# Optimization experiments

Hardware: AMD Instinct MI355X
Metric: run time of the kernel (lower is better)

Reference implementation:

```python
import jax, jax.numpy as jnp
import numpy as np

C = 512
HEADS = 8
HEAD_DIM = 64
OUT = 2560
NEG = -1.0e12
EPS = 1e-5


def _layernorm(x, g, b):
    mu = jnp.mean(x, axis=-1, keepdims=True)
    var = jnp.mean(jnp.square(x - mu), axis=-1, keepdims=True)
    return (x - mu) * jax.lax.rsqrt(var + EPS) * g + b


def setup_inputs() -> dict:
    key = jax.random.key(0)
    ks = jax.random.split(key, 16)
    s = 0.02
    return {
        "x": jax.random.normal(ks[0], (8, C, 32, 32), dtype=jnp.float32),
        "conv_w": jax.random.normal(ks[1], (C, C), dtype=jnp.float32) * s,
        "conv_b": jnp.zeros((C,), jnp.float32),
        "ln_g": jnp.ones((C,), jnp.float32),
        "ln_b": jnp.zeros((C,), jnp.float32),
        "qkv_w": jax.random.normal(ks[2], (3 * C, C), dtype=jnp.float32) * s,
        "qkv_b": jnp.zeros((3 * C,), jnp.float32),
        "proj_w": jax.random.normal(ks[3], (C, C), dtype=jnp.float32) * s,
        "proj_b": jnp.zeros((C,), jnp.float32),
        "w1": jax.random.normal(ks[4], (C, C), dtype=jnp.float32) * s,
        "b1": jnp.zeros((C,), jnp.float32),
        "w2": jax.random.normal(ks[5], (C, C), dtype=jnp.float32) * s,
        "b2": jnp.zeros((C,), jnp.float32),
        "fc_w": jax.random.normal(ks[6], (OUT, C), dtype=jnp.float32) * s,
        "fc_b": jnp.zeros((OUT,), jnp.float32),
    }


def reference(x, conv_w, conv_b, ln_g, ln_b, qkv_w, qkv_b, proj_w, proj_b,
              w1, b1, w2, b2, fc_w, fc_b):
    B, Cc, H, W = x.shape
    N = H * W
    mk = jax.random.split(jax.random.key(42), 3)

    # Flat1D: conv1x1 == per-pixel linear, then flatten -> [B, N, C]
    t = jnp.einsum('bchw,oc->bhwo', x, conv_w) + conv_b
    t = t.reshape(B, N, Cc)

    # LayerNorm (shared params)
    t = _layernorm(t, ln_g, ln_b)

    # Attention with random additive mask (p=0.5)
    qkv = t @ qkv_w.T + qkv_b  # [B, N, 3C]
    qkv = qkv.reshape(B, N, 3, HEADS, Cc // HEADS)
    q = jnp.transpose(qkv[:, :, 0], (0, 2, 1, 3))  # [B, H, N, D]
    k = jnp.transpose(qkv[:, :, 1], (0, 2, 1, 3))
    v = jnp.transpose(qkv[:, :, 2], (0, 2, 1, 3))
    scale = HEAD_DIM ** (-0.5)
    attn = jnp.einsum('bhnd,bhmd->bhnm', q, k) * scale
    amask = jax.random.bernoulli(mk[0], 0.5, attn.shape)
    attn = attn + amask.astype(attn.dtype) * NEG
    attn = jax.nn.softmax(attn, axis=-1)
    o = jnp.einsum('bhnm,bhmd->bhnd', attn, v)
    o = jnp.transpose(o, (0, 2, 1, 3)).reshape(B, N, Cc)
    t = o @ proj_w.T + proj_b

    # FeedForward with random additive masks
    h = jax.nn.gelu(t @ w1.T + b1, approximate=False)
    m1 = jax.random.bernoulli(mk[1], 0.3, h.shape)
    h = h + m1.astype(h.dtype) * NEG
    t = h @ w2.T + b2
    m2 = jax.random.bernoulli(mk[2], 0.1, t.shape)
    t = t + m2.astype(t.dtype) * NEG

    # LayerNorm (same params), mean over tokens, final fc
    t = _layernorm(t, ln_g, ln_b)
    t = jnp.mean(t, axis=1)  # [B, C]
    return t @ fc_w.T + fc_b
```

## Files before the change

### kernel.cpp

```cpp
#include <hip/hip_runtime.h>
#include <stdint.h>
#include <math.h>

#define NEGV -1.0e12f
#define QSCALE 0.18033688011112042f

typedef __attribute__((ext_vector_type(8))) short bf16x8;
typedef __attribute__((ext_vector_type(4))) float f32x4;
typedef __attribute__((ext_vector_type(8))) ushort u16x8;

#define ROTL1(v, r) ({ uint32_t _d;                                            \
    asm("v_alignbit_b32 %0, %1, %1, %2" : "=v"(_d) : "v"(v), "n"(32 - (r)));   \
    _d; })

#if defined(__has_builtin)
#if __has_builtin(__builtin_amdgcn_exp2f)
#define EXP2(x) __builtin_amdgcn_exp2f(x)
#endif
#endif
#ifndef EXP2
#define EXP2(x) exp2f(x)
#endif

__host__ static void tf2x32_host(uint32_t k0, uint32_t k1, uint32_t c0, uint32_t c1,
                                 uint32_t* o0, uint32_t* o1) {
    uint32_t ks2 = k0 ^ k1 ^ 0x1BD11BDAu;
    uint32_t x0 = c0 + k0, x1 = c1 + k1;
#define TF_RND(r) x0 += x1; x1 = ((x1 << (r)) | (x1 >> (32 - (r)))); x1 ^= x0;
    TF_RND(13) TF_RND(15) TF_RND(26) TF_RND(6)
    x0 += k1;  x1 += ks2 + 1u;
    TF_RND(17) TF_RND(29) TF_RND(16) TF_RND(24)
    x0 += ks2; x1 += k0 + 2u;
    TF_RND(13) TF_RND(15) TF_RND(26) TF_RND(6)
    x0 += k0;  x1 += k1 + 3u;
    TF_RND(17) TF_RND(29) TF_RND(16) TF_RND(24)
    x0 += k1;  x1 += ks2 + 4u;
    TF_RND(13) TF_RND(15) TF_RND(26) TF_RND(6)
    x0 += ks2; x1 += k0 + 5u;
#undef TF_RND
    *o0 = x0; *o1 = x1;
}

__device__ __forceinline__ uint32_t tf_bits(uint32_t k0, uint32_t k1, uint32_t j) {
    const uint32_t ks2 = k0 ^ k1 ^ 0x1BD11BDAu;
    uint32_t x0 = k0, x1 = j + k1;
#define TFR(r) x0 += x1; x1 = ROTL1(x1, r); x1 ^= x0;
    TFR(13) TFR(15) TFR(26) TFR(6)
    x0 += k1;  x1 += ks2 + 1u;
    TFR(17) TFR(29) TFR(16) TFR(24)
    x0 += ks2; x1 += k0 + 2u;
    TFR(13) TFR(15) TFR(26) TFR(6)
    x0 += k0;  x1 += k1 + 3u;
    TFR(17) TFR(29) TFR(16) TFR(24)
    x0 += k1;  x1 += ks2 + 4u;
    TFR(13) TFR(15) TFR(26) TFR(6)
#undef TFR
    return (x0 + ks2) ^ (x1 + (k0 + 5u));
}

__host__ static uint32_t maskT(float p) {
    double t = ceil((double)p * 8388608.0);
    return ((uint32_t)t) << 9;
}

__device__ __forceinline__ ushort f2bf(float x) {
    uint32_t u = __float_as_uint(x);
    u += 0x7fffu + ((u >> 16) & 1u);
    return (ushort)(u >> 16);
}
__device__ __forceinline__ float bf2f(ushort u) {
    return __uint_as_float(((uint32_t)u) << 16);
}

__global__ __launch_bounds__(256) void prep_k(const float* __restrict__ x,
                                              ushort* __restrict__ xt,
                                              const float* __restrict__ s0,
                                              const float* __restrict__ s1,
                                              const float* __restrict__ s2,
                                              const float* __restrict__ s3,
                                              const float* __restrict__ s4,
                                              ushort* __restrict__ wdst)
{
    __shared__ float tile[64][65];
    const int tid = threadIdx.x;
    if (blockIdx.x < 1024) {
        const int id = blockIdx.x;
        const int n0 = (id & 15) * 64, c0 = ((id >> 4) & 7) * 64, b = id >> 7;
        const float* src = x + ((size_t)b * 512 + c0) * 1024 + n0;
#pragma unroll
        for (int i = 0; i < 4; ++i) {
            const int r = (tid >> 4) + i * 16;
            const int col = (tid & 15) * 4;
            float4 v = *(const float4*)(src + (size_t)r * 1024 + col);
            tile[r][col + 0] = v.x; tile[r][col + 1] = v.y;
            tile[r][col + 2] = v.z; tile[r][col + 3] = v.w;
        }
        __syncthreads();
#pragma unroll
        for (int i = 0; i < 2; ++i) {
            const int nl = (tid >> 3) + i * 32;
            const int cb = (tid & 7) * 8;
            u16x8 o;
#pragma unroll
            for (int j = 0; j < 8; ++j) o[j] = f2bf(tile[cb + j][nl]);
            *(u16x8*)(xt + ((size_t)b * 1024 + n0 + nl) * 512 + c0 + cb) = o;
        }
    } else {
        const size_t i = ((size_t)(blockIdx.x - 1024) * 256 + tid) * 8;
        const float* src; size_t off;
        if (i < 262144)       { src = s0; off = 0; }
        else if (i < 1048576) { src = s1; off = 262144; }
        else if (i < 1310720) { src = s2; off = 1048576; }
        else if (i < 1572864) { src = s3; off = 1310720; }
        else                  { src = s4; off = 1572864; }
        const float* p = src + (i - off);
        float4 a = *(const float4*)p;
        float4 b = *(const float4*)(p + 4);
        u16x8 o;
        o[0] = f2bf(a.x); o[1] = f2bf(a.y); o[2] = f2bf(a.z); o[3] = f2bf(a.w);
        o[4] = f2bf(b.x); o[5] = f2bf(b.y); o[6] = f2bf(b.z); o[7] = f2bf(b.w);
        *(u16x8*)(wdst + i) = o;
    }
}

template<int EPI>
__global__ __launch_bounds__(256) void bgemm_k(
    const ushort* __restrict__ A, const ushort* __restrict__ W,
    const float* __restrict__ bias, float* __restrict__ outf,
    ushort* __restrict__ outb,
    ushort* __restrict__ qb, ushort* __restrict__ kb, ushort* __restrict__ vb,
    uint32_t mkk0, uint32_t mkk1, uint32_t T)
{
    const int tid = threadIdx.x;
    const int wave = tid >> 6, lane = tid & 63;
    const int lg = lane >> 4, lc = lane & 15;
    const int m0 = blockIdx.x * 128 + wave * 32;
    const int o0 = blockIdx.y * 64;

    f32x4 acc[2][4];
#pragma unroll
    for (int i = 0; i < 2; ++i)
#pragma unroll
        for (int j = 0; j < 4; ++j) acc[i][j] = (f32x4){0.f, 0.f, 0.f, 0.f};

    const ushort* Ab = A + (size_t)(m0 + lc) * 512 + lg * 8;
    const ushort* Wb = W + (size_t)(o0 + lc) * 512 + lg * 8;

#pragma unroll 4
    for (int k0 = 0; k0 < 512; k0 += 32) {
        bf16x8 aq[2], bw[4];
        aq[0] = *(const bf16x8*)(Ab + k0);
        aq[1] = *(const bf16x8*)(Ab + 16 * 512 + k0);
#pragma unroll
        for (int j = 0; j < 4; ++j) bw[j] = *(const bf16x8*)(Wb + (size_t)j * 16 * 512 + k0);
#pragma unroll
        for (int i = 0; i < 2; ++i)
#pragma unroll
            for (int j = 0; j < 4; ++j)
                acc[i][j] = __builtin_amdgcn_mfma_f32_16x16x32_bf16(aq[i], bw[j], acc[i][j], 0, 0, 0);
    }

    float bvv[4];
#pragma unroll
    for (int j = 0; j < 4; ++j) bvv[j] = bias[o0 + j * 16 + lc];

#pragma unroll
    for (int i = 0; i < 2; ++i) {
#pragma unroll
        for (int j = 0; j < 4; ++j) {
#pragma unroll
            for (int r = 0; r < 4; ++r) {
                const int m = m0 + i * 16 + lg * 4 + r;
                const int o = o0 + j * 16 + lc;
                float v = acc[i][j][r] + bvv[j];
                if constexpr (EPI == 4) {
                    outb[(size_t)m * 512 + o] = f2bf(v);
                } else if constexpr (EPI == 2) {
                    v = 0.5f * v * (1.0f + erff(v * 0.70710678118654752f));
                    if (tf_bits(mkk0, mkk1, (uint32_t)(m * 512 + o)) < T) v += NEGV;
                    outb[(size_t)m * 512 + o] = f2bf(v);
                } else if constexpr (EPI == 3) {
                    if (tf_bits(mkk0, mkk1, (uint32_t)(m * 512 + o)) < T) v += NEGV;
                    outf[(size_t)m * 512 + o] = v;
                } else {
                    const int s = o >> 9, hh = (o >> 6) & 7, d = o & 63;
                    const int b = m >> 10, n = m & 1023;
                    const int bh = b * 8 + hh;
                    ushort* dst = (s == 0) ? qb : (s == 1) ? kb : vb;
                    const float scl = (s == 0) ? QSCALE : 1.0f;
                    dst[((size_t)bh * 1024 + n) * 64 + d] = f2bf(v * scl);
                }
            }
        }
    }
}

__global__ __launch_bounds__(256) void vxpose_k(const ushort* __restrict__ v,
                                                ushort* __restrict__ vt)
{
    __shared__ ushort tile[64][72];
    const int tid = threadIdx.x;
    const int bh = blockIdx.y, n0 = blockIdx.x * 64;
    const int row = tid >> 2, cq = (tid & 3) * 16;
    const ushort* src = v + ((size_t)bh * 1024 + n0 + row) * 64 + cq;
    *(u16x8*)&tile[row][cq] = *(const u16x8*)src;
    *(u16x8*)&tile[row][cq + 8] = *(const u16x8*)(src + 8);
    __syncthreads();
    const int d = tid >> 2, nq = (tid & 3) * 16;
    u16x8 o0v, o1v;
#pragma unroll
    for (int i = 0; i < 8; ++i) o0v[i] = tile[nq + i][d];
#pragma unroll
    for (int i = 0; i < 8; ++i) o1v[i] = tile[nq + 8 + i][d];
    ushort* dst = vt + ((size_t)bh * 64 + d) * 1024 + n0 + nq;
    *(u16x8*)dst = o0v;
    *(u16x8*)(dst + 8) = o1v;
}

__global__ __launch_bounds__(256) void ln_k(const ushort* __restrict__ in,
                                            const float* __restrict__ g,
                                            const float* __restrict__ bb,
                                            ushort* __restrict__ outb)
{
    const int wave = threadIdx.x >> 6, lane = threadIdx.x & 63;
    const size_t tok = (size_t)blockIdx.x * 4 + wave;
    const ushort* row = in + tok * 512;
    const int c0 = lane * 8;
    u16x8 vv = *(const u16x8*)(row + c0);
    float x[8];
#pragma unroll
    for (int i = 0; i < 8; i++) x[i] = bf2f(vv[i]);
    float s = 0.f;
#pragma unroll
    for (int i = 0; i < 8; i++) s += x[i];
#pragma unroll
    for (int sh = 32; sh; sh >>= 1) s += __shfl_xor(s, sh, 64);
    const float mu = s * (1.0f / 512.0f);
    float vsum = 0.f;
#pragma unroll
    for (int i = 0; i < 8; i++) { float d = x[i] - mu; vsum += d * d; }
#pragma unroll
    for (int sh = 32; sh; sh >>= 1) vsum += __shfl_xor(vsum, sh, 64);
    const float inv = 1.0f / sqrtf(vsum * (1.0f / 512.0f) + 1e-5f);
    float4 g0 = *(const float4*)(g + c0);
    float4 g1 = *(const float4*)(g + c0 + 4);
    float4 b0 = *(const float4*)(bb + c0);
    float4 b1 = *(const float4*)(bb + c0 + 4);
    float gg[8] = {g0.x, g0.y, g0.z, g0.w, g1.x, g1.y, g1.z, g1.w};
    float bv[8] = {b0.x, b0.y, b0.z, b0.w, b1.x, b1.y, b1.z, b1.w};
    u16x8 o;
#pragma unroll
    for (int i = 0; i < 8; i++) o[i] = f2bf((x[i] - mu) * inv * gg[i] + bv[i]);
    *(u16x8*)(outb + tok * 512 + c0) = o;
}

__global__ __launch_bounds__(256) void ln2mean_k(const float* __restrict__ in,
                                                 const float* __restrict__ g,
                                                 const float* __restrict__ bb,
                                                 float* __restrict__ pblock)
{
    __shared__ float rows[4][512];
    const int wave = threadIdx.x >> 6, lane = threadIdx.x & 63;
    const int b = blockIdx.x >> 8;
    const size_t tok = (size_t)b * 1024 + (blockIdx.x & 255) * 4 + wave;
    const float* row = in + tok * 512;
    const int c0 = lane * 8;
    float4 v0 = *(const float4*)(row + c0);
    float4 v1 = *(const float4*)(row + c0 + 4);
    float x[8] = {v0.x, v0.y, v0.z, v0.w, v1.x, v1.y, v1.z, v1.w};
    float s = 0.f;
#pragma unroll
    for (int i = 0; i < 8; i++) s += x[i];
#pragma unroll
    for (int sh = 32; sh; sh >>= 1) s += __shfl_xor(s, sh, 64);
    const float mu = s * (1.0f / 512.0f);
    float vsum = 0.f;
#pragma unroll
    for (int i = 0; i < 8; i++) { float d = x[i] - mu; vsum += d * d; }
#pragma unroll
    for (int sh = 32; sh; sh >>= 1) vsum += __shfl_xor(vsum, sh, 64);
    const float inv = 1.0f / sqrtf(vsum * (1.0f / 512.0f) + 1e-5f);
    float4 g0 = *(const float4*)(g + c0);
    float4 g1 = *(const float4*)(g + c0 + 4);
    float4 b0 = *(const float4*)(bb + c0);
    float4 b1 = *(const float4*)(bb + c0 + 4);
    float gg[8] = {g0.x, g0.y, g0.z, g0.w, g1.x, g1.y, g1.z, g1.w};
    float bv[8] = {b0.x, b0.y, b0.z, b0.w, b1.x, b1.y, b1.z, b1.w};
    float o[8];
#pragma unroll
    for (int i = 0; i < 8; i++) o[i] = (x[i] - mu) * inv * gg[i] + bv[i];
    *(float4*)&rows[wave][c0]     = make_float4(o[0], o[1], o[2], o[3]);
    *(float4*)&rows[wave][c0 + 4] = make_float4(o[4], o[5], o[6], o[7]);
    __syncthreads();
    const int c = threadIdx.x;
    float p0 = rows[0][c] + rows[1][c] + rows[2][c] + rows[3][c];
    float p1 = rows[0][c + 256] + rows[1][c + 256] + rows[2][c + 256] + rows[3][c + 256];
    pblock[(size_t)blockIdx.x * 512 + c] = p0;
    pblock[(size_t)blockIdx.x * 512 + c + 256] = p1;
}

__global__ __launch_bounds__(256) void mred_k(const float* __restrict__ pblock,
                                              float* __restrict__ tm)
{
    __shared__ float red[8][33];
    const int c0 = blockIdx.x * 32, b = blockIdx.y;
    const int cl = threadIdx.x & 31, jg = threadIdx.x >> 5;
    const float* p = pblock + ((size_t)b * 256 + jg * 32) * 512 + c0 + cl;
    float s = 0.f;
#pragma unroll 8
    for (int j = 0; j < 32; ++j) s += p[(size_t)j * 512];
    red[jg][cl] = s;
    __syncthreads();
    if (jg == 0) {
        float t = 0.f;
#pragma unroll
        for (int g2 = 0; g2 < 8; ++g2) t += red[g2][cl];
        tm[b * 512 + c0 + cl] = t * (1.0f / 1024.0f);
    }
}

__global__ __launch_bounds__(256) void attn_k(
    const ushort* __restrict__ qb, const ushort* __restrict__ kb,
    const ushort* __restrict__ vtb, ushort* __restrict__ ob,
    uint32_t km0, uint32_t km1)
{
    __shared__ ushort plds[4][16][40];
    const int tid = threadIdx.x;
    const int wave = tid >> 6, lane = tid & 63;
    const int bh = blockIdx.x & 63;
    const int qt = blockIdx.x >> 6;
    const int b = bh >> 3, h = bh & 7;
    const int q0 = qt * 64 + wave * 16;
    const int lg = lane >> 4, lc = lane & 15;

    const ushort* qp = qb + (size_t)bh * 65536;

    bf16x8 aq0 = *(const bf16x8*)(qp + (size_t)(q0 + lc) * 64 + lg * 8);
    bf16x8 aq1 = *(const bf16x8*)(qp + (size_t)(q0 + lc) * 64 + 32 + lg * 8);

    f32x4 zero = {0.f, 0.f, 0.f, 0.f};
    f32x4 oacc[4] = {zero, zero, zero, zero};
    float D[4] = {0.f, 0.f, 0.f, 0.f};

    uint32_t jr[4];
#pragma unroll
    for (int r = 0; r < 4; ++r)
        jr[r] = ((uint32_t)bh * 1024u + (uint32_t)(q0 + lg * 4 + r)) * 1024u + (uint32_t)lc;

    const ushort* krow = kb + (size_t)bh * 65536 + (size_t)lc * 64 + lg * 8;
    const ushort* vrow = vtb + (size_t)bh * 65536 + (size_t)lc * 1024 + lg * 8;

    for (int ch = 0; ch < 32; ++ch) {
        bf16x8 bk00 = *(const bf16x8*)(krow);
        bf16x8 bk01 = *(const bf16x8*)(krow + 32);
        bf16x8 bk10 = *(const bf16x8*)(krow + 1024);
        bf16x8 bk11 = *(const bf16x8*)(krow + 1056);

        f32x4 s0 = __builtin_amdgcn_mfma_f32_16x16x32_bf16(aq0, bk00, zero, 0, 0, 0);
        s0 = __builtin_amdgcn_mfma_f32_16x16x32_bf16(aq1, bk01, s0, 0, 0, 0);
        f32x4 s1 = __builtin_amdgcn_mfma_f32_16x16x32_bf16(aq0, bk10, zero, 0, 0, 0);
        s1 = __builtin_amdgcn_mfma_f32_16x16x32_bf16(aq1, bk11, s1, 0, 0, 0);

#pragma unroll
        for (int r = 0; r < 4; ++r) {
            const uint32_t bits0 = tf_bits(km0, km1, jr[r]);
            const uint32_t bits1 = tf_bits(km0, km1, jr[r] + 16u);
            jr[r] += 32u;
            const float pv0 = ((int)bits0 < 0) ? EXP2(s0[r]) : 0.f;
            const float pv1 = ((int)bits1 < 0) ? EXP2(s1[r]) : 0.f;
            D[r] += pv0 + pv1;
            uint32_t pk;
            asm("v_cvt_pk_bf16_f32 %0, %1, %2" : "=v"(pk) : "v"(pv0), "v"(pv1));
            plds[wave][lg * 4 + r][lc] = (ushort)pk;
            plds[wave][lg * 4 + r][lc + 16] = (ushort)(pk >> 16);
        }

        bf16x8 pa = *(const bf16x8*)&plds[wave][lc][lg * 8];

#pragma unroll
        for (int dt = 0; dt < 4; ++dt) {
            bf16x8 bv = *(const bf16x8*)(vrow + (size_t)dt * 16384);
            oacc[dt] = __builtin_amdgcn_mfma_f32_16x16x32_bf16(pa, bv, oacc[dt], 0, 0, 0);
        }
        krow += 2048;
        vrow += 32;
    }

#pragma unroll
    for (int r = 0; r < 4; ++r) {
#pragma unroll
        for (int sh = 1; sh < 16; sh <<= 1) D[r] += __shfl_xor(D[r], sh, 64);
    }

#pragma unroll
    for (int r = 0; r < 4; ++r) {
        const int q = q0 + lg * 4 + r;
        const float inv = 1.0f / D[r];
        ushort* orow = ob + ((size_t)b * 1024 + q) * 512 + h * 64;
#pragma unroll
        for (int dt = 0; dt < 4; ++dt) orow[dt * 16 + lc] = f2bf(oacc[dt][r] * inv);
    }
}

__global__ __launch_bounds__(256) void fc_k(const float* __restrict__ tm,
                                            const float* __restrict__ w,
                                            const float* __restrict__ bias,
                                            float* __restrict__ outp)
{
    const int b = blockIdx.y;
    const int o = blockIdx.x * 256 + threadIdx.x;
    const float* tr = tm + b * 512;
    const float* wr = w + (size_t)o * 512;
    float s = 0.f;
    for (int k = 0; k < 512; k += 4) {
        float4 a = *(const float4*)(tr + k);
        float4 ww = *(const float4*)(wr + k);
        s = fmaf(a.x, ww.x, s); s = fmaf(a.y, ww.y, s);
        s = fmaf(a.z, ww.z, s); s = fmaf(a.w, ww.w, s);
    }
    outp[b * 2560 + o] = s + bias[o];
}

extern "C" void kernel_launch(void* const* d_in, const int* in_sizes, int n_in,
                              void* d_out, int out_size, void* d_ws, size_t ws_size,
                              hipStream_t stream)
{
    const float* x      = (const float*)d_in[0];
    const float* conv_w = (const float*)d_in[1];
    const float* conv_b = (const float*)d_in[2];
    const float* ln_g   = (const float*)d_in[3];
    const float* ln_b   = (const float*)d_in[4];
    const float* qkv_w  = (const float*)d_in[5];
    const float* qkv_b  = (const float*)d_in[6];
    const float* proj_w = (const float*)d_in[7];
    const float* proj_b = (const float*)d_in[8];
    const float* w1     = (const float*)d_in[9];
    const float* b1     = (const float*)d_in[10];
    const float* w2     = (const float*)d_in[11];
    const float* b2     = (const float*)d_in[12];
    const float* fc_w   = (const float*)d_in[13];
    const float* fc_b   = (const float*)d_in[14];
    float* out = (float*)d_out;

    if (ws_size < (size_t)71303168) return;

    uint32_t mk0a, mk0b, mk1a, mk1b, mk2a, mk2b;
    tf2x32_host(0u, 42u, 0u, 0u, &mk0a, &mk0b);
    tf2x32_host(0u, 42u, 0u, 1u, &mk1a, &mk1b);
    tf2x32_host(0u, 42u, 0u, 2u, &mk2a, &mk2b);
    const uint32_t T_m1 = maskT(0.3f);
    const uint32_t T_m2 = maskT(0.1f);

    char* wsb = (char*)d_ws;
    ushort* xt     = (ushort*)wsb;
    ushort* wts    = (ushort*)(wsb + 8388608);
    ushort* qbuf   = (ushort*)(wsb + 12582912);
    ushort* kbuf   = (ushort*)(wsb + 20971520);
    ushort* vbuf   = (ushort*)(wsb + 29360128);
    ushort* vtbuf  = (ushort*)(wsb + 37748736);
    ushort* convbf = (ushort*)(wsb + 46137344);
    float*  t2     = (float*)(wsb + 46137344);
    ushort* ln1bf  = (ushort*)(wsb + 62914560);
    ushort* obuf   = xt;
    ushort* projbf = ln1bf;
    ushort* hbuf   = qbuf;
    float*  pblock = (float*)(wsb + 20971520);
    float*  tm     = (float*)(wsb + 25165824);

    ushort* wconv = wts;
    ushort* wqkv  = wts + 262144;
    ushort* wproj = wts + 1048576;
    ushort* ww1   = wts + 1310720;
    ushort* ww2   = wts + 1572864;

    dim3 blk(256);
    prep_k<<<dim3(1920), blk, 0, stream>>>(x, xt, conv_w, qkv_w, proj_w, w1, w2, wts);
    bgemm_k<4><<<dim3(64, 8), blk, 0, stream>>>(xt, wconv, conv_b, nullptr, convbf,
                                                nullptr, nullptr, nullptr, 0u, 0u, 0u);
    ln_k<<<dim3(2048), blk, 0, stream>>>(convbf, ln_g, ln_b, ln1bf);
    bgemm_k<1><<<dim3(64, 24), blk, 0, stream>>>(ln1bf, wqkv, qkv_b, nullptr, nullptr,
                                                 qbuf, kbuf, vbuf, 0u, 0u, 0u);
    vxpose_k<<<dim3(16, 64), blk, 0, stream>>>(vbuf, vtbuf);
    attn_k<<<dim3(1024), blk, 0, stream>>>(qbuf, kbuf, vtbuf, obuf, mk0a, mk0b);
    bgemm_k<4><<<dim3(64, 8), blk, 0, stream>>>(obuf, wproj, proj_b, nullptr, projbf,
                                                nullptr, nullptr, nullptr, 0u, 0u, 0u);
    bgemm_k<2><<<dim3(64, 8), blk, 0, stream>>>(projbf, ww1, b1, nullptr, hbuf,
                                                nullptr, nullptr, nullptr, mk1a, mk1b, T_m1);
    bgemm_k<3><<<dim3(64, 8), blk, 0, stream>>>(hbuf, ww2, b2, t2, nullptr,
                                                nullptr, nullptr, nullptr, mk2a, mk2b, T_m2);
    ln2mean_k<<<dim3(2048), blk, 0, stream>>>(t2, ln_g, ln_b, pblock);
    mred_k<<<dim3(16, 8), blk, 0, stream>>>(pblock, tm);
    fc_k<<<dim3(10, 8), blk, 0, stream>>>(tm, fc_w, fc_b, out);
}
```

Baseline: 357.5 us.

## Fuse attention, proj, FFN, second layernorm and token-mean into one kernel

```diff
diff --git a/kernel.cpp b/kernel.cpp
--- a/kernel.cpp
+++ b/kernel.cpp
@@ -126,10 +126,9 @@
 template<int EPI>
 __global__ __launch_bounds__(256) void bgemm_k(
     const ushort* __restrict__ A, const ushort* __restrict__ W,
-    const float* __restrict__ bias, float* __restrict__ outf,
+    const float* __restrict__ bias,
     ushort* __restrict__ outb,
-    ushort* __restrict__ qb, ushort* __restrict__ kb, ushort* __restrict__ vb,
-    uint32_t mkk0, uint32_t mkk1, uint32_t T)
+    ushort* __restrict__ qb, ushort* __restrict__ kb, ushort* __restrict__ vb)
 {
     const int tid = threadIdx.x;
     const int wave = tid >> 6, lane = tid & 63;
@@ -175,13 +174,6 @@
                 float v = acc[i][j][r] + bvv[j];
                 if constexpr (EPI == 4) {
                     outb[(size_t)m * 512 + o] = f2bf(v);
-                } else if constexpr (EPI == 2) {
-                    v = 0.5f * v * (1.0f + erff(v * 0.70710678118654752f));
-                    if (tf_bits(mkk0, mkk1, (uint32_t)(m * 512 + o)) < T) v += NEGV;
-                    outb[(size_t)m * 512 + o] = f2bf(v);
-                } else if constexpr (EPI == 3) {
-                    if (tf_bits(mkk0, mkk1, (uint32_t)(m * 512 + o)) < T) v += NEGV;
-                    outf[(size_t)m * 512 + o] = v;
                 } else {
                     const int s = o >> 9, hh = (o >> 6) & 7, d = o & 63;
                     const int b = m >> 10, n = m & 1023;
@@ -254,87 +246,28 @@
     *(u16x8*)(outb + tok * 512 + c0) = o;
 }
 
-__global__ __launch_bounds__(256) void ln2mean_k(const float* __restrict__ in,
-                                                 const float* __restrict__ g,
-                                                 const float* __restrict__ bb,
-                                                 float* __restrict__ pblock)
-{
-    __shared__ float rows[4][512];
-    const int wave = threadIdx.x >> 6, lane = threadIdx.x & 63;
-    const int b = blockIdx.x >> 8;
-    const size_t tok = (size_t)b * 1024 + (blockIdx.x & 255) * 4 + wave;
-    const float* row = in + tok * 512;
-    const int c0 = lane * 8;
-    float4 v0 = *(const float4*)(row + c0);
-    float4 v1 = *(const float4*)(row + c0 + 4);
-    float x[8] = {v0.x, v0.y, v0.z, v0.w, v1.x, v1.y, v1.z, v1.w};
-    float s = 0.f;
-#pragma unroll
-    for (int i = 0; i < 8; i++) s += x[i];
-#pragma unroll
-    for (int sh = 32; sh; sh >>= 1) s += __shfl_xor(s, sh, 64);
-    const float mu = s * (1.0f / 512.0f);
-    float vsum = 0.f;
-#pragma unroll
-    for (int i = 0; i < 8; i++) { float d = x[i] - mu; vsum += d * d; }
-#pragma unroll
-    for (int sh = 32; sh; sh >>= 1) vsum += __shfl_xor(vsum, sh, 64);
-    const float inv = 1.0f / sqrtf(vsum * (1.0f / 512.0f) + 1e-5f);
-    float4 g0 = *(const float4*)(g + c0);
-    float4 g1 = *(const float4*)(g + c0 + 4);
-    float4 b0 = *(const float4*)(bb + c0);
-    float4 b1 = *(const float4*)(bb + c0 + 4);
-    float gg[8] = {g0.x, g0.y, g0.z, g0.w, g1.x, g1.y, g1.z, g1.w};
-    float bv[8] = {b0.x, b0.y, b0.z, b0.w, b1.x, b1.y, b1.z, b1.w};
-    float o[8];
-#pragma unroll
-    for (int i = 0; i < 8; i++) o[i] = (x[i] - mu) * inv * gg[i] + bv[i];
-    *(float4*)&rows[wave][c0]     = make_float4(o[0], o[1], o[2], o[3]);
-    *(float4*)&rows[wave][c0 + 4] = make_float4(o[4], o[5], o[6], o[7]);
-    __syncthreads();
-    const int c = threadIdx.x;
-    float p0 = rows[0][c] + rows[1][c] + rows[2][c] + rows[3][c];
-    float p1 = rows[0][c + 256] + rows[1][c + 256] + rows[2][c + 256] + rows[3][c + 256];
-    pblock[(size_t)blockIdx.x * 512 + c] = p0;
-    pblock[(size_t)blockIdx.x * 512 + c + 256] = p1;
-}
-
-__global__ __launch_bounds__(256) void mred_k(const float* __restrict__ pblock,
-                                              float* __restrict__ tm)
-{
-    __shared__ float red[8][33];
-    const int c0 = blockIdx.x * 32, b = blockIdx.y;
-    const int cl = threadIdx.x & 31, jg = threadIdx.x >> 5;
-    const float* p = pblock + ((size_t)b * 256 + jg * 32) * 512 + c0 + cl;
-    float s = 0.f;
-#pragma unroll 8
-    for (int j = 0; j < 32; ++j) s += p[(size_t)j * 512];
-    red[jg][cl] = s;
-    __syncthreads();
-    if (jg == 0) {
-        float t = 0.f;
-#pragma unroll
-        for (int g2 = 0; g2 < 8; ++g2) t += red[g2][cl];
-        tm[b * 512 + c0 + cl] = t * (1.0f / 1024.0f);
-    }
-}
-
-__global__ __launch_bounds__(256) void attn_k(
+__global__ __launch_bounds__(512) void mega_k(
     const ushort* __restrict__ qb, const ushort* __restrict__ kb,
-    const ushort* __restrict__ vtb, ushort* __restrict__ ob,
-    uint32_t km0, uint32_t km1)
-{
-    __shared__ ushort plds[4][16][40];
+    const ushort* __restrict__ vtb,
+    const ushort* __restrict__ wproj, const float* __restrict__ pjb,
+    const ushort* __restrict__ ww1, const float* __restrict__ b1v,
+    const ushort* __restrict__ ww2, const float* __restrict__ b2v,
+    const float* __restrict__ g, const float* __restrict__ bln,
+    float* __restrict__ pblock,
+    uint32_t km0, uint32_t km1, uint32_t k10, uint32_t k11,
+    uint32_t k20, uint32_t k21, uint32_t T1, uint32_t T2)
+{
+    __shared__ ushort bufA[16][520];
+    __shared__ ushort plds[8][16][40];
+    __shared__ float stats[16][8][2];
     const int tid = threadIdx.x;
     const int wave = tid >> 6, lane = tid & 63;
-    const int bh = blockIdx.x & 63;
-    const int qt = blockIdx.x >> 6;
-    const int b = bh >> 3, h = bh & 7;
-    const int q0 = qt * 64 + wave * 16;
     const int lg = lane >> 4, lc = lane & 15;
+    const int b = blockIdx.x & 7, tg = blockIdx.x >> 3;
+    const int bh = b * 8 + wave;
+    const int q0 = tg * 16;
 
     const ushort* qp = qb + (size_t)bh * 65536;
-
     bf16x8 aq0 = *(const bf16x8*)(qp + (size_t)(q0 + lc) * 64 + lg * 8);
     bf16x8 aq1 = *(const bf16x8*)(qp + (size_t)(q0 + lc) * 64 + 32 + lg * 8);
 
@@ -394,12 +327,166 @@
 
 #pragma unroll
     for (int r = 0; r < 4; ++r) {
-        const int q = q0 + lg * 4 + r;
+        const int row = lg * 4 + r;
         const float inv = 1.0f / D[r];
-        ushort* orow = ob + ((size_t)b * 1024 + q) * 512 + h * 64;
-#pragma unroll
-        for (int dt = 0; dt < 4; ++dt) orow[dt * 16 + lc] = f2bf(oacc[dt][r] * inv);
-    }
+#pragma unroll
+        for (int dt = 0; dt < 4; ++dt)
+            bufA[row][wave * 64 + dt * 16 + lc] = f2bf(oacc[dt][r] * inv);
+    }
+    __syncthreads();
+
+    const int o0 = wave * 64;
+    const int mg0 = b * 1024 + tg * 16 + lg * 4;
+
+    f32x4 acc[4] = {zero, zero, zero, zero};
+    {
+        const ushort* Wb = wproj + (size_t)(o0 + lc) * 512 + lg * 8;
+#pragma unroll 4
+        for (int k0 = 0; k0 < 512; k0 += 32) {
+            bf16x8 a0 = *(const bf16x8*)&bufA[lc][k0 + lg * 8];
+#pragma unroll
+            for (int j = 0; j < 4; ++j) {
+                bf16x8 bw = *(const bf16x8*)(Wb + (size_t)j * 16 * 512 + k0);
+                acc[j] = __builtin_amdgcn_mfma_f32_16x16x32_bf16(a0, bw, acc[j], 0, 0, 0);
+            }
+        }
+    }
+    float bias4[4];
+#pragma unroll
+    for (int j = 0; j < 4; ++j) bias4[j] = pjb[o0 + j * 16 + lc];
+    __syncthreads();
+#pragma unroll
+    for (int j = 0; j < 4; ++j)
+#pragma unroll
+        for (int r = 0; r < 4; ++r)
+            bufA[lg * 4 + r][o0 + j * 16 + lc] = f2bf(acc[j][r] + bias4[j]);
+    __syncthreads();
+
+#pragma unroll
+    for (int j = 0; j < 4; ++j) acc[j] = zero;
+    {
+        const ushort* Wb = ww1 + (size_t)(o0 + lc) * 512 + lg * 8;
+#pragma unroll 4
+        for (int k0 = 0; k0 < 512; k0 += 32) {
+            bf16x8 a0 = *(const bf16x8*)&bufA[lc][k0 + lg * 8];
+#pragma unroll
+            for (int j = 0; j < 4; ++j) {
+                bf16x8 bw = *(const bf16x8*)(Wb + (size_t)j * 16 * 512 + k0);
+                acc[j] = __builtin_amdgcn_mfma_f32_16x16x32_bf16(a0, bw, acc[j], 0, 0, 0);
+            }
+        }
+    }
+#pragma unroll
+    for (int j = 0; j < 4; ++j) bias4[j] = b1v[o0 + j * 16 + lc];
+    __syncthreads();
+#pragma unroll
+    for (int j = 0; j < 4; ++j) {
+#pragma unroll
+        for (int r = 0; r < 4; ++r) {
+            float v = acc[j][r] + bias4[j];
+            v = 0.5f * v * (1.0f + erff(v * 0.70710678118654752f));
+            const uint32_t jidx = (uint32_t)((mg0 + r) * 512 + o0 + j * 16 + lc);
+            if (tf_bits(k10, k11, jidx) < T1) v += NEGV;
+            bufA[lg * 4 + r][o0 + j * 16 + lc] = f2bf(v);
+        }
+    }
+    __syncthreads();
+
+#pragma unroll
+    for (int j = 0; j < 4; ++j) acc[j] = zero;
+    {
+        const ushort* Wb = ww2 + (size_t)(o0 + lc) * 512 + lg * 8;
+#pragma unroll 4
+        for (int k0 = 0; k0 < 512; k0 += 32) {
+            bf16x8 a0 = *(const bf16x8*)&bufA[lc][k0 + lg * 8];
+#pragma unroll
+            for (int j = 0; j < 4; ++j) {
+                bf16x8 bw = *(const bf16x8*)(Wb + (size_t)j * 16 * 512 + k0);
+                acc[j] = __builtin_amdgcn_mfma_f32_16x16x32_bf16(a0, bw, acc[j], 0, 0, 0);
+            }
+        }
+    }
+#pragma unroll
+    for (int j = 0; j < 4; ++j) bias4[j] = b2v[o0 + j * 16 + lc];
+    float t2v[4][4];
+#pragma unroll
+    for (int j = 0; j < 4; ++j) {
+#pragma unroll
+        for (int r = 0; r < 4; ++r) {
+            float v = acc[j][r] + bias4[j];
+            const uint32_t jidx = (uint32_t)((mg0 + r) * 512 + o0 + j * 16 + lc);
+            if (tf_bits(k20, k21, jidx) < T2) v += NEGV;
+            t2v[j][r] = v;
+        }
+    }
+
+    float rs[4], rq[4];
+#pragma unroll
+    for (int r = 0; r < 4; ++r) {
+        float s = 0.f, q = 0.f;
+#pragma unroll
+        for (int j = 0; j < 4; ++j) { s += t2v[j][r]; q += t2v[j][r] * t2v[j][r]; }
+#pragma unroll
+        for (int sh = 1; sh < 16; sh <<= 1) {
+            s += __shfl_xor(s, sh, 64);
+            q += __shfl_xor(q, sh, 64);
+        }
+        rs[r] = s; rq[r] = q;
+    }
+    if (lc == 0) {
+#pragma unroll
+        for (int r = 0; r < 4; ++r) {
+            stats[lg * 4 + r][wave][0] = rs[r];
+            stats[lg * 4 + r][wave][1] = rq[r];
+        }
+    }
+    __syncthreads();
+    float mu[4], inv[4];
+#pragma unroll
+    for (int r = 0; r < 4; ++r) {
+        float S = 0.f, S2 = 0.f;
+#pragma unroll
+        for (int w = 0; w < 8; ++w) { S += stats[lg * 4 + r][w][0]; S2 += stats[lg * 4 + r][w][1]; }
+        const float m = S * (1.0f / 512.0f);
+        const float var = S2 * (1.0f / 512.0f) - m * m;
+        mu[r] = m;
+        inv[r] = 1.0f / sqrtf(var + 1e-5f);
+    }
+    float gld[4], bld[4];
+#pragma unroll
+    for (int j = 0; j < 4; ++j) {
+        gld[j] = g[o0 + j * 16 + lc];
+        bld[j] = bln[o0 + j * 16 + lc];
+    }
+    float ps[4] = {0.f, 0.f, 0.f, 0.f};
+#pragma unroll
+    for (int j = 0; j < 4; ++j) {
+#pragma unroll
+        for (int r = 0; r < 4; ++r)
+            ps[j] += (t2v[j][r] - mu[r]) * inv[r] * gld[j] + bld[j];
+    }
+#pragma unroll
+    for (int j = 0; j < 4; ++j) {
+        ps[j] += __shfl_xor(ps[j], 16, 64);
+        ps[j] += __shfl_xor(ps[j], 32, 64);
+    }
+    if (lg == 0) {
+#pragma unroll
+        for (int j = 0; j < 4; ++j)
+            pblock[((size_t)(b * 64 + tg)) * 512 + o0 + j * 16 + lc] = ps[j];
+    }
+}
+
+__global__ __launch_bounds__(256) void mred2_k(const float* __restrict__ pblock,
+                                               float* __restrict__ tm)
+{
+    const int b = blockIdx.y;
+    const int c = blockIdx.x * 256 + threadIdx.x;
+    const float* p = pblock + (size_t)b * 64 * 512 + c;
+    float s = 0.f;
+#pragma unroll 8
+    for (int t = 0; t < 64; ++t) s += p[(size_t)t * 512];
+    tm[b * 512 + c] = s * (1.0f / 1024.0f);
 }
 
 __global__ __launch_bounds__(256) void fc_k(const float* __restrict__ tm,
@@ -459,13 +546,9 @@
     ushort* vbuf   = (ushort*)(wsb + 29360128);
     ushort* vtbuf  = (ushort*)(wsb + 37748736);
     ushort* convbf = (ushort*)(wsb + 46137344);
-    float*  t2     = (float*)(wsb + 46137344);
-    ushort* ln1bf  = (ushort*)(wsb + 62914560);
-    ushort* obuf   = xt;
-    ushort* projbf = ln1bf;
-    ushort* hbuf   = qbuf;
-    float*  pblock = (float*)(wsb + 20971520);
-    float*  tm     = (float*)(wsb + 25165824);
+    ushort* ln1bf  = (ushort*)(wsb + 54525952);
+    float*  pblock = (float*)(wsb + 62914560);
+    float*  tm     = (float*)(wsb + 64487424);
 
     ushort* wconv = wts;
     ushort* wqkv  = wts + 262144;
@@ -475,20 +558,17 @@
 
     dim3 blk(256);
     prep_k<<<dim3(1920), blk, 0, stream>>>(x, xt, conv_w, qkv_w, proj_w, w1, w2, wts);
-    bgemm_k<4><<<dim3(64, 8), blk, 0, stream>>>(xt, wconv, conv_b, nullptr, convbf,
-                                                nullptr, nullptr, nullptr, 0u, 0u, 0u);
+    bgemm_k<4><<<dim3(64, 8), blk, 0, stream>>>(xt, wconv, conv_b, convbf,
+                                                nullptr, nullptr, nullptr);
     ln_k<<<dim3(2048), blk, 0, stream>>>(convbf, ln_g, ln_b, ln1bf);
-    bgemm_k<1><<<dim3(64, 24), blk, 0, stream>>>(ln1bf, wqkv, qkv_b, nullptr, nullptr,
-                                                 qbuf, kbuf, vbuf, 0u, 0u, 0u);
+    bgemm_k<1><<<dim3(64, 24), blk, 0, stream>>>(ln1bf, wqkv, qkv_b, nullptr,
+                                                 qbuf, kbuf, vbuf);
     vxpose_k<<<dim3(16, 64), blk, 0, stream>>>(vbuf, vtbuf);
-    attn_k<<<dim3(1024), blk, 0, stream>>>(qbuf, kbuf, vtbuf, obuf, mk0a, mk0b);
-    bgemm_k<4><<<dim3(64, 8), blk, 0, stream>>>(obuf, wproj, proj_b, nullptr, projbf,
-                                                nullptr, nullptr, nullptr, 0u, 0u, 0u);
-    bgemm_k<2><<<dim3(64, 8), blk, 0, stream>>>(projbf, ww1, b1, nullptr, hbuf,
-                                                nullptr, nullptr, nullptr, mk1a, mk1b, T_m1);
-    bgemm_k<3><<<dim3(64, 8), blk, 0, stream>>>(hbuf, ww2, b2, t2, nullptr,
-                                                nullptr, nullptr, nullptr, mk2a, mk2b, T_m2);
-    ln2mean_k<<<dim3(2048), blk, 0, stream>>>(t2, ln_g, ln_b, pblock);
-    mred_k<<<dim3(16, 8), blk, 0, stream>>>(pblock, tm);
+    mega_k<<<dim3(512), dim3(512), 0, stream>>>(qbuf, kbuf, vtbuf,
+                                                wproj, proj_b, ww1, b1, ww2, b2,
+                                                ln_g, ln_b, pblock,
+                                                mk0a, mk0b, mk1a, mk1b, mk2a, mk2b,
+                                                T_m1, T_m2);
+    mred2_k<<<dim3(2, 8), blk, 0, stream>>>(pblock, tm);
     fc_k<<<dim3(10, 8), blk, 0, stream>>>(tm, fc_w, fc_b, out);
 }
```

After: 354.2 us. About the same (-0.9%).
